# Kernel tuning notes

Hardware: AMD Instinct MI355X
Metric: run time of the kernel (lower is better)

The kernel has to match this reference:

```python
import jax, jax.numpy as jnp
import numpy as np

B, T, D_IN, H, D_ENC, P, D_ATT = 64, 20, 512, 512, 2048, 196, 512


def setup_inputs() -> dict:
    key = jax.random.key(0)
    ks = jax.random.split(key, 12)
    s = 0.05  # weight scale to keep gates out of saturation
    return {
        "x": jax.random.normal(ks[0], (B, T, D_IN), jnp.float32),
        "cnn_features": jax.random.normal(ks[1], (B, P, D_ENC), jnp.float32),
        "Wi": jax.random.normal(ks[2], (D_IN + H + D_ENC, H), jnp.float32) * s,
        "bi": jnp.zeros((H,), jnp.float32),
        "Wf": jax.random.normal(ks[3], (D_IN + H + D_ENC, H), jnp.float32) * s,
        "bf": jnp.zeros((H,), jnp.float32),
        "Wc": jax.random.normal(ks[4], (D_IN + H + D_ENC, H), jnp.float32) * s,
        "bc": jnp.zeros((H,), jnp.float32),
        "Wo": jax.random.normal(ks[5], (D_IN + H + D_ENC, H), jnp.float32) * s,
        "bo": jnp.zeros((H,), jnp.float32),
        "Wa_feat": jax.random.normal(ks[6], (D_ENC, D_ATT), jnp.float32) * s,
        "Wa_h": jax.random.normal(ks[7], (H, D_ATT), jnp.float32) * s,
        "ba": jnp.zeros((D_ATT,), jnp.float32),
        "v": jax.random.normal(ks[8], (D_ATT,), jnp.float32) * s,
    }


def reference(x, cnn_features, Wi, bi, Wf, bf, Wc, bc, Wo, bo, Wa_feat, Wa_h, ba, v):
    batch, seq_len, _ = x.shape
    hid = Wi.shape[1]
    # feature projection is h-independent: hoist out of the time loop
    feat_proj = jnp.einsum('bpe,ea->bpa', cnn_features, Wa_feat) + ba  # [B,P,A]

    def step(carry, x_t):
        h, c = carry
        # additive (Bahdanau) attention over pixels
        e = jnp.einsum('bpa,a->bp', jnp.tanh(feat_proj + (h @ Wa_h)[:, None, :]), v)
        alpha = jax.nn.softmax(e, axis=-1)                      # [B,P]
        ctx = jnp.einsum('bp,bpe->be', alpha, cnn_features)     # [B,E]
        comb = jnp.concatenate([x_t, h, ctx], axis=1)           # [B,D_IN+H+E]
        i_t = jax.nn.sigmoid(comb @ Wi + bi)
        f_t = jax.nn.sigmoid(comb @ Wf + bf)
        o_t = jax.nn.sigmoid(comb @ Wo + bo)
        c_tilde = jnp.tanh(comb @ Wc + bc)
        c_new = f_t * c + i_t * c_tilde
        h_new = o_t * jnp.tanh(c_new)
        return (h_new, c_new), h_new

    h0 = jnp.zeros((batch, hid), x.dtype)
    c0 = jnp.zeros((batch, hid), x.dtype)
    (h_T, c_T), ys = jax.lax.scan(step, (h0, c0), jnp.swapaxes(x, 0, 1))
    outputs = jnp.swapaxes(ys, 0, 1)  # [B,T,H]
    return outputs, h_T, c_T
```

## Files before the change

kernel.cpp:

```cpp
#include <hip/hip_runtime.h>

typedef unsigned short u16;
typedef unsigned int u32;
typedef __attribute__((ext_vector_type(8))) short bf16x8;
typedef __attribute__((ext_vector_type(4))) float f32x4;

#define NB 64
#define NT 20
#define NH 512
#define NP 196
#define NE 2048
#define NA 512

__device__ __forceinline__ u16 f2bf(float f) {
  u32 b = __float_as_uint(f);
  return (u16)((b + 0x7FFFu + ((b >> 16) & 1u)) >> 16);
}
__device__ __forceinline__ float bf2f(u16 u) { return __uint_as_float(((u32)u) << 16); }
__device__ __forceinline__ float tanh_fast(float x) {
  float xc = fminf(fmaxf(x, -15.f), 15.f);
  float e2 = __builtin_amdgcn_exp2f(xc * 2.885390082f);
  return (e2 - 1.f) * __builtin_amdgcn_rcpf(e2 + 1.f);
}
__device__ __forceinline__ float sigmoid_fast(float x) {
  return __builtin_amdgcn_rcpf(1.f + __builtin_amdgcn_exp2f(x * -1.44269504f));
}

__device__ __forceinline__ void gload_lds16(const u16* g, u16* l) {
  __builtin_amdgcn_global_load_lds((const __attribute__((address_space(1))) void*)g,
                                   (__attribute__((address_space(3))) void*)l, 16, 0, 0);
}

template <int N>
__device__ __forceinline__ void vwait() {
  if constexpr (N >= 0)
    asm volatile("s_waitcnt vmcnt(%0)" ::"i"(N) : "memory");
  else
    asm volatile("" ::: "memory");
}

__global__ __launch_bounds__(256) void conv_bf16(const float4* __restrict__ src,
                                                 u16* __restrict__ dst, int n4) {
  int i = blockIdx.x * 256 + threadIdx.x;
  int stride = gridDim.x * 256;
  for (; i < n4; i += stride) {
    float4 v = src[i];
    u32 lo = (u32)f2bf(v.x) | ((u32)f2bf(v.y) << 16);
    u32 hi = (u32)f2bf(v.z) | ((u32)f2bf(v.w) << 16);
    *(uint2*)(dst + (size_t)i * 4) = make_uint2(lo, hi);
  }
}

__global__ __launch_bounds__(128) void conv_x(const float* __restrict__ x,
                                              u16* __restrict__ xbT) {
  int b = blockIdx.x, t = blockIdx.y, tid = threadIdx.x;
  float4 v = *(const float4*)(x + ((size_t)b * NT + t) * 512 + tid * 4);
  u32 lo = (u32)f2bf(v.x) | ((u32)f2bf(v.y) << 16);
  u32 hi = (u32)f2bf(v.z) | ((u32)f2bf(v.w) << 16);
  *(uint2*)(xbT + ((size_t)t * NB + b) * 512 + tid * 4) = make_uint2(lo, hi);
}

__global__ __launch_bounds__(256) void transpose_w(const float* __restrict__ W0,
                                                   const float* __restrict__ W1,
                                                   const float* __restrict__ W2,
                                                   const float* __restrict__ W3,
                                                   u16* __restrict__ dst, int row_off, int K) {
  const float* src = blockIdx.z == 0 ? W0 : blockIdx.z == 1 ? W1 : blockIdx.z == 2 ? W2 : W3;
  __shared__ float tile[32][33];
  int k0 = blockIdx.x * 32, n0 = blockIdx.y * 32;
  int tx = threadIdx.x & 31, ty = threadIdx.x >> 5;
#pragma unroll
  for (int i = 0; i < 4; ++i)
    tile[ty + i * 8][tx] = src[(size_t)(row_off + k0 + ty + i * 8) * 512 + n0 + tx];
  __syncthreads();
#pragma unroll
  for (int i = 0; i < 4; ++i) {
    int n = n0 + ty + i * 8, k = k0 + tx;
    dst[((size_t)blockIdx.z * 512 + n) * K + k] = f2bf(tile[tx][ty + i * 8]);
  }
}

__global__ __launch_bounds__(256) void gemm_bf16(const u16* __restrict__ A,
                                                 const u16* __restrict__ BT,
                                                 float* __restrict__ C, int M, int N, int K) {
  __shared__ u16 lA[128 * 64];
  __shared__ u16 lB[128 * 64];
  const int tid = threadIdx.x;
  const int lane = tid & 63;
  const int wid = tid >> 6;
  const int m0 = blockIdx.x * 128, n0 = blockIdx.y * 128;
  const int wm = (wid >> 1) * 64, wn = (wid & 1) * 64;
  f32x4 acc[4][4] = {};

  const int cbase = wid * 256;
  int srcr[4], srcc[4];
#pragma unroll
  for (int it = 0; it < 4; ++it) {
    int c = cbase + it * 64 + lane;
    srcr[it] = c >> 3;
    srcc[it] = ((c & 7) ^ ((c >> 3) & 7)) * 8;
  }

  for (int k0 = 0; k0 < K; k0 += 64) {
    __syncthreads();
#pragma unroll
    for (int it = 0; it < 4; ++it) {
      gload_lds16(A + (size_t)(m0 + srcr[it]) * K + k0 + srcc[it],
                  lA + (size_t)(cbase + it * 64) * 8);
      gload_lds16(BT + (size_t)(n0 + srcr[it]) * K + k0 + srcc[it],
                  lB + (size_t)(cbase + it * 64) * 8);
    }
    __syncthreads();
#pragma unroll
    for (int kk = 0; kk < 2; ++kk) {
      int kchunk = kk * 4 + (lane >> 4);
      bf16x8 af[4], bg[4];
#pragma unroll
      for (int i = 0; i < 4; ++i) {
        int row = wm + i * 16 + (lane & 15);
        af[i] = *(const bf16x8*)(lA + row * 64 + ((kchunk ^ (row & 7)) * 8));
        int rowb = wn + i * 16 + (lane & 15);
        bg[i] = *(const bf16x8*)(lB + rowb * 64 + ((kchunk ^ (rowb & 7)) * 8));
      }
#pragma unroll
      for (int i = 0; i < 4; ++i)
#pragma unroll
        for (int j = 0; j < 4; ++j)
          acc[i][j] = __builtin_amdgcn_mfma_f32_16x16x32_bf16(af[i], bg[j], acc[i][j], 0, 0, 0);
    }
  }
#pragma unroll
  for (int i = 0; i < 4; ++i) {
    int m = m0 + wm + i * 16 + ((lane >> 4) * 4);
#pragma unroll
    for (int j = 0; j < 4; ++j) {
      int n = n0 + wn + j * 16 + (lane & 15);
#pragma unroll
      for (int r = 0; r < 4; ++r) C[(size_t)(m + r) * N + n] = acc[i][j][r];
    }
  }
}

#define STG(SS, CUR, K1)                                                                    \
  do {                                                                                      \
    _Pragma("unroll") for (int q_ = 0; q_ < 2; ++q_) {                                      \
      const u16* g_ = ((SS) < 2)                                                            \
                          ? (A + (size_t)(m0 + sR[SS][q_]) * K + (K1) + sC[SS][q_])         \
                          : (BT + (size_t)(n0 + sR[SS][q_]) * K + (K1) + sC[SS][q_]);       \
      gload_lds16(g_, lds + ((CUR) ^ 1) * 32768 + sL[SS][q_]);                              \
    }                                                                                       \
  } while (0)

#define PH(MF0, READB, CUR, DOSTAGE, SB, K1, WN)                                            \
  do {                                                                                      \
    const u16* pA_ = lds + (CUR) * 32768;                                                   \
    const u16* pB_ = pA_ + 16384;                                                           \
    bf16x8 af_[2][2];                                                                       \
    _Pragma("unroll") for (int kh_ = 0; kh_ < 2; ++kh_) {                                   \
      const int kc_ = kh_ * 4 + (lane >> 4);                                                \
      _Pragma("unroll") for (int ii_ = 0; ii_ < 2; ++ii_) {                                 \
        const int rA_ = wmH * 128 + ((MF0) + ii_) * 16 + l15;                               \
        af_[kh_][ii_] = *(const bf16x8*)(pA_ + rA_ * 64 + ((kc_ ^ (rA_ & 7)) * 8));         \
      }                                                                                     \
      if (READB) {                                                                          \
        _Pragma("unroll") for (int j_ = 0; j_ < 4; ++j_) {                                  \
          const int rB_ = wnq * 64 + j_ * 16 + l15;                                         \
          bg[kh_][j_] = *(const bf16x8*)(pB_ + rB_ * 64 + ((kc_ ^ (rB_ & 7)) * 8));         \
        }                                                                                   \
      }                                                                                     \
    }                                                                                       \
    if (DOSTAGE) {                                                                          \
      STG(SB, CUR, K1);                                                                     \
      STG((SB) + 1, CUR, K1);                                                               \
    }                                                                                       \
    vwait<WN>();                                                                            \
    __builtin_amdgcn_s_barrier();                                                           \
    __builtin_amdgcn_s_setprio(1);                                                          \
    _Pragma("unroll") for (int kh_ = 0; kh_ < 2; ++kh_)                                     \
      _Pragma("unroll") for (int ii_ = 0; ii_ < 2; ++ii_)                                   \
        _Pragma("unroll") for (int j_ = 0; j_ < 4; ++j_)                                    \
          acc[(MF0) + ii_][j_] = __builtin_amdgcn_mfma_f32_16x16x32_bf16(                   \
              af_[kh_][ii_], bg[kh_][j_], acc[(MF0) + ii_][j_], 0, 0, 0);                   \
    __builtin_amdgcn_s_setprio(0);                                                          \
    __builtin_amdgcn_s_barrier();                                                           \
  } while (0)

__global__ __launch_bounds__(512, 2) void gemm256(const u16* __restrict__ A,
                                                  const u16* __restrict__ BT,
                                                  const float* __restrict__ bias,
                                                  u16* __restrict__ fpb, u16* __restrict__ cnW,
                                                  int K, int grid_n) {
  __shared__ u16 lds[65536];
  const int tid = threadIdx.x;
  const int lane = tid & 63;
  const int wid = tid >> 6;
  const int l15 = lane & 15;
  const int nblk = gridDim.x;
  const int q = nblk >> 3, rr = nblk & 7;
  const int xcd = blockIdx.x & 7, jj = blockIdx.x >> 3;
  const int swz = (xcd < rr ? xcd * (q + 1) : rr * (q + 1) + (xcd - rr) * q) + jj;
  const int mt = swz / grid_n, nt = swz - mt * grid_n;
  const int m0 = mt * 256, n0 = nt * 256;
  const int wmH = wid >> 2;
  const int wnq = wid & 3;
  f32x4 acc[8][4] = {};
  bf16x8 bg[2][4];

  int sR[4][2], sC[4][2], sL[4][2];
#pragma unroll
  for (int s = 0; s < 4; ++s)
#pragma unroll
    for (int qq = 0; qq < 2; ++qq) {
      int reg = (s < 2) ? s : s - 2;
      int ra = reg * 1024 + qq * 512 + wid * 64;
      int idx = ra + lane;
      sR[s][qq] = idx >> 3;
      sC[s][qq] = ((idx & 7) ^ ((idx >> 3) & 7)) * 8;
      sL[s][qq] = ((s < 2) ? 0 : 16384) + ra * 8;
    }

  STG(0, 1, 0);
  STG(1, 1, 0);
  STG(2, 1, 0);
  STG(3, 1, 0);
  vwait<0>();
  __builtin_amdgcn_s_barrier();

  const int KT = K >> 6;
  for (int kt = 0; kt < KT - 1; ++kt) {
    const int cur = kt & 1;
    const int k1 = (kt + 1) << 6;
    PH(0, 1, cur, 1, 0, k1, -1);
    PH(2, 0, cur, 1, 2, k1, -1);
    PH(4, 0, cur, 0, 0, 0, -1);
    PH(6, 0, cur, 0, 0, 0, 0);
  }
  {
    const int cur = (KT - 1) & 1;
    PH(0, 1, cur, 0, 0, 0, -1);
    PH(2, 0, cur, 0, 0, 0, -1);
    PH(4, 0, cur, 0, 0, 0, -1);
    PH(6, 0, cur, 0, 0, 0, -1);
  }

#pragma unroll
  for (int i = 0; i < 8; ++i) {
    int m = m0 + wmH * 128 + i * 16 + ((lane >> 4) * 4);
#pragma unroll
    for (int j = 0; j < 4; ++j) {
      int n = n0 + wnq * 64 + j * 16 + l15;
      float bv = (n < 512) ? bias[n] : 0.f;
#pragma unroll
      for (int r = 0; r < 4; ++r) {
        float val = acc[i][j][r] + bv;
        u32 me = (u32)(m + r);
        if (n < 512) {
          fpb[(size_t)me * 512 + n] = f2bf(val);
        } else {
          u32 bdx = me / 196u;
          u32 p = me - bdx * 196u;
          u32 g = (u32)(n - 512) >> 9;
          u32 n9 = (u32)(n - 512) & 511u;
          cnW[(((size_t)bdx * 4 + g) * 196 + p) * 512 + n9] = f2bf(val);
        }
      }
    }
  }
}

__global__ __launch_bounds__(256) void hproj(const u16* __restrict__ hprev,
                                             const u16* __restrict__ wcT,
                                             float* __restrict__ hp) {
  const int ntile = blockIdx.x;
  const int tid = threadIdx.x, lane = tid & 63, kh = tid >> 6;
  const int l15 = lane & 15;
  const u16* Bp = wcT + (size_t)(ntile * 16 + l15) * 512 + kh * 128 + ((lane >> 4) * 8);
  const u16* Ap = hprev + (size_t)l15 * 512 + kh * 128 + ((lane >> 4) * 8);
  f32x4 acc[4] = {};
#pragma unroll
  for (int ks = 0; ks < 4; ++ks) {
    bf16x8 bb = *(const bf16x8*)(Bp + ks * 32);
#pragma unroll
    for (int mf = 0; mf < 4; ++mf) {
      bf16x8 a = *(const bf16x8*)(Ap + (size_t)mf * 16 * 512 + ks * 32);
      acc[mf] = __builtin_amdgcn_mfma_f32_16x16x32_bf16(a, bb, acc[mf], 0, 0, 0);
    }
  }
  __shared__ float pre[4][64][16];
  const int rrow = (lane >> 4) * 4;
#pragma unroll
  for (int mf = 0; mf < 4; ++mf)
#pragma unroll
    for (int r = 0; r < 4; ++r) pre[kh][mf * 16 + rrow + r][l15] = acc[mf][r];
  __syncthreads();
  const int m = tid >> 2, n = (tid & 3) * 4;
  float4 s;
  float* sp = (float*)&s;
#pragma unroll
  for (int j = 0; j < 4; ++j)
    sp[j] = pre[0][m][n + j] + pre[1][m][n + j] + pre[2][m][n + j] + pre[3][m][n + j];
  *(float4*)(hp + (size_t)m * 2560 + ntile * 16 + n) = s;
}

__global__ __launch_bounds__(1024) void attn_gates(
    const u16* __restrict__ fpb, const float* __restrict__ hp, const float* __restrict__ v,
    const u16* __restrict__ cw, const float* __restrict__ xw, const float* __restrict__ bi,
    const float* __restrict__ bfg, const float* __restrict__ bc, const float* __restrict__ bo,
    float* __restrict__ cbuf, float* __restrict__ out, u16* __restrict__ hnext, int t) {
  const int b = blockIdx.x & 63;
  const int quarter = blockIdx.x >> 6;
  const int tid = threadIdx.x;
  const int lane = tid & 63, wid = tid >> 6;
  __shared__ float smem_a[1024];
  __shared__ float sm[16];
  __shared__ float alp[200];
  __shared__ float red[8192];

  float* hwa = smem_a;
  float* vv = smem_a + 512;
  if (tid < 512) {
    hwa[tid] = (t > 0) ? hp[(size_t)b * 2560 + 2048 + tid] : 0.f;
    vv[tid] = v[tid];
  }
  if (tid >= 196 && tid < 256) red[tid] = -3e38f;
  __syncthreads();

  float hw[8], vr[8];
#pragma unroll
  for (int j = 0; j < 8; ++j) {
    hw[j] = hwa[lane * 8 + j];
    vr[j] = vv[lane * 8 + j];
  }
  for (int p = wid; p < NP; p += 16) {
    const u16* fp = fpb + ((size_t)b * NP + p) * 512 + lane * 8;
    uint4 raw = *(const uint4*)fp;
    u32 w[4] = {raw.x, raw.y, raw.z, raw.w};
    float part = 0.f;
#pragma unroll
    for (int j = 0; j < 8; ++j) {
      u16 u = (u16)(w[j >> 1] >> ((j & 1) * 16));
      part += tanh_fast(bf2f(u) + hw[j]) * vr[j];
    }
#pragma unroll
    for (int off = 32; off > 0; off >>= 1) part += __shfl_xor(part, off);
    if (lane == 0) red[p] = part;
  }
  __syncthreads();

  float ev = 0.f, w = 0.f;
  if (tid < 256) {
    ev = red[tid];
    float m_ = ev;
#pragma unroll
    for (int off = 32; off > 0; off >>= 1) m_ = fmaxf(m_, __shfl_xor(m_, off));
    if (lane == 0) sm[wid] = m_;
  }
  __syncthreads();
  if (tid < 256) {
    float mx = fmaxf(fmaxf(sm[0], sm[1]), fmaxf(sm[2], sm[3]));
    w = (tid < NP) ? __builtin_amdgcn_exp2f((ev - mx) * 1.44269504f) : 0.f;
    float s_ = w;
#pragma unroll
    for (int off = 32; off > 0; off >>= 1) s_ += __shfl_xor(s_, off);
    if (lane == 0) sm[8 + wid] = s_;
  }
  __syncthreads();
  if (tid < NP) {
    float tot = (sm[8] + sm[9]) + (sm[10] + sm[11]);
    alp[tid] = w * __builtin_amdgcn_rcpf(tot);
  }
  __syncthreads();

  {
    const int g = tid >> 8, pg = (tid >> 4) & 15, colc = tid & 15;
    const u16* base = cw + ((size_t)(b * 4 + g) * 196) * 512 + quarter * 128 + colc * 8;
    float acc[8] = {};
    for (int i = 0; i < 13; ++i) {
      int p = pg + i * 16;
      if (p < NP) {
        float al = alp[p];
        uint4 raw = *(const uint4*)(base + (size_t)p * 512);
        u32 wds[4] = {raw.x, raw.y, raw.z, raw.w};
#pragma unroll
        for (int j = 0; j < 8; ++j) acc[j] += al * bf2f((u16)(wds[j >> 1] >> ((j & 1) * 16)));
      }
    }
#pragma unroll
    for (int j = 0; j < 8; ++j) red[((g * 16 + pg) * 16 + colc) * 8 + j] = acc[j];
  }
  __syncthreads();

  float* pre4 = smem_a;
  if (tid < 512) {
    const int g = tid >> 7, nn = tid & 127;
    float s = 0.f;
#pragma unroll
    for (int pg = 0; pg < 16; ++pg) s += red[((g * 16 + pg) * 16 + (nn >> 3)) * 8 + (nn & 7)];
    pre4[g * 128 + nn] = s;
  }
  __syncthreads();

  if (tid < 128) {
    const int ng = quarter * 128 + tid;
    const size_t xwo = ((size_t)t * NB + b) * 2048;
    const size_t hpb = (size_t)b * 2560;
    float hwh0 = 0.f, hwh1 = 0.f, hwh2 = 0.f, hwh3 = 0.f;
    if (t > 0) {
      hwh0 = hp[hpb + ng];
      hwh1 = hp[hpb + 512 + ng];
      hwh2 = hp[hpb + 1024 + ng];
      hwh3 = hp[hpb + 1536 + ng];
    }
    float ip = pre4[0 * 128 + tid] + xw[xwo + ng] + hwh0 + bi[ng];
    float fp = pre4[1 * 128 + tid] + xw[xwo + 512 + ng] + hwh1 + bfg[ng];
    float cp = pre4[2 * 128 + tid] + xw[xwo + 1024 + ng] + hwh2 + bc[ng];
    float op = pre4[3 * 128 + tid] + xw[xwo + 1536 + ng] + hwh3 + bo[ng];
    float it = sigmoid_fast(ip), ft = sigmoid_fast(fp), ot = sigmoid_fast(op);
    float ctl = tanh_fast(cp);
    float cold = (t > 0) ? cbuf[(size_t)b * 512 + ng] : 0.f;
    float cn = ft * cold + it * ctl;
    float hn = ot * tanh_fast(cn);
    cbuf[(size_t)b * 512 + ng] = cn;
    hnext[(size_t)b * 512 + ng] = f2bf(hn);
    out[((size_t)b * NT + t) * 512 + ng] = hn;
    if (t == NT - 1) {
      out[(size_t)NB * NT * 512 + (size_t)b * 512 + ng] = hn;
      out[(size_t)NB * NT * 512 + (size_t)NB * 512 + (size_t)b * 512 + ng] = cn;
    }
  }
}

extern "C" void kernel_launch(void* const* d_in, const int* in_sizes, int n_in, void* d_out,
                              int out_size, void* d_ws, size_t ws_size, hipStream_t stream) {
  const float* x = (const float*)d_in[0];
  const float* cnn = (const float*)d_in[1];
  const float* Wi = (const float*)d_in[2];
  const float* bi = (const float*)d_in[3];
  const float* Wf = (const float*)d_in[4];
  const float* bfv = (const float*)d_in[5];
  const float* Wc = (const float*)d_in[6];
  const float* bc = (const float*)d_in[7];
  const float* Wo = (const float*)d_in[8];
  const float* bo = (const float*)d_in[9];
  const float* Waf = (const float*)d_in[10];
  const float* Wah = (const float*)d_in[11];
  const float* ba = (const float*)d_in[12];
  const float* v = (const float*)d_in[13];
  float* out = (float*)d_out;

  char* base = (char*)d_ws;
  size_t off = 0;
  auto alloc = [&](size_t bytes) {
    char* r = base + off;
    off += (bytes + 255) & ~(size_t)255;
    return r;
  };
  u16* cnnb = (u16*)alloc((size_t)NB * NP * NE * 2);
  u16* fpb = (u16*)alloc((size_t)NB * NP * NA * 2);
  u16* cnW = (u16*)alloc((size_t)NB * 4 * NP * 512 * 2);
  u16* wbig = (u16*)alloc((size_t)2560 * 2048 * 2);
  u16* wcombT = (u16*)alloc((size_t)2560 * 512 * 2);
  u16* wxt = (u16*)alloc((size_t)4 * 512 * 512 * 2);
  u16* xbT = (u16*)alloc((size_t)NT * NB * 512 * 2);
  float* xw = (float*)alloc((size_t)NT * NB * 2048 * 4);
  u16* hbuf = (u16*)alloc((size_t)2 * NB * 512 * 2);
  float* cbuf = (float*)alloc((size_t)NB * 512 * 4);
  float* hp = (float*)alloc((size_t)NB * 2560 * 4);

  (void)ws_size;
  (void)in_sizes;
  (void)n_in;
  (void)out_size;

  conv_bf16<<<2048, 256, 0, stream>>>((const float4*)cnn, cnnb, (NB * NP * NE) / 4);
  conv_x<<<dim3(NB, NT), 128, 0, stream>>>(x, xbT);
  {
    dim3 g1(512 / 32, 16, 4);
    transpose_w<<<g1, 256, 0, stream>>>(Wi, Wf, Wc, Wo, wxt, 0, 512);
    dim3 g2(2048 / 32, 16, 1);
    transpose_w<<<g2, 256, 0, stream>>>(Waf, Waf, Waf, Waf, wbig, 0, 2048);
    dim3 g3(2048 / 32, 16, 4);
    transpose_w<<<g3, 256, 0, stream>>>(Wi, Wf, Wc, Wo, wbig + (size_t)512 * 2048, 1024, 2048);
    dim3 g4(512 / 32, 16, 4);
    transpose_w<<<g4, 256, 0, stream>>>(Wi, Wf, Wc, Wo, wcombT, 512, 512);
    dim3 g5(512 / 32, 16, 1);
    transpose_w<<<g5, 256, 0, stream>>>(Wah, Wah, Wah, Wah, wcombT + (size_t)2048 * 512, 0, 512);
  }

  gemm256<<<49 * 10, 512, 0, stream>>>(cnnb, wbig, ba, fpb, cnW, 2048, 10);

  {
    dim3 g(1280 / 128, 2048 / 128);
    gemm_bf16<<<g, 256, 0, stream>>>(xbT, wxt, xw, 1280, 2048, 512);
  }

  for (int t = 0; t < NT; ++t) {
    const u16* hprev = hbuf + (size_t)(t & 1) * NB * 512;
    u16* hnext = hbuf + (size_t)((t + 1) & 1) * NB * 512;
    if (t > 0) hproj<<<160, 256, 0, stream>>>(hprev, wcombT, hp);
    attn_gates<<<256, 1024, 0, stream>>>(fpb, hp, v, cnW, xw, bi, bfv, bc, bo, cbuf, out, hnext,
                                         t);
  }
}
```

Measured before the change: 672.5 us.

## Triple-buffer A tiles and single-buffer B in gemm256 LDS pipeline

The gemm256 LDS staging moves from double-buffered A and B to a three-slot ring for A plus one B slot. A tiles are now prefetched two k-steps ahead, and B for the next step is loaded into the single slot after its fragments are read into registers in the first phase. The aim is deeper prefetch of A without growing LDS, which could hide more global-load latency. In exchange the vmcnt accounting and barrier ordering are more intricate, and the ring needs extra peeled tail iterations.

```diff
diff --git a/kernel.cpp b/kernel.cpp
--- a/kernel.cpp
+++ b/kernel.cpp
@@ -141,20 +141,26 @@
   }
 }
 
-#define STG(SS, CUR, K1)                                                                    \
+#define STGA(ABASE, K1)                                                                     \
   do {                                                                                      \
-    _Pragma("unroll") for (int q_ = 0; q_ < 2; ++q_) {                                      \
-      const u16* g_ = ((SS) < 2)                                                            \
-                          ? (A + (size_t)(m0 + sR[SS][q_]) * K + (K1) + sC[SS][q_])         \
-                          : (BT + (size_t)(n0 + sR[SS][q_]) * K + (K1) + sC[SS][q_]);       \
-      gload_lds16(g_, lds + ((CUR) ^ 1) * 32768 + sL[SS][q_]);                              \
-    }                                                                                       \
+    _Pragma("unroll") for (int s_ = 0; s_ < 2; ++s_)                                        \
+        _Pragma("unroll") for (int q_ = 0; q_ < 2; ++q_)                                    \
+            gload_lds16(A + (size_t)(m0 + sR[s_][q_]) * K + (K1) + sC[s_][q_],              \
+                        lds + (ABASE) + sL[s_][q_]);                                        \
   } while (0)
 
-#define PH(MF0, READB, CUR, DOSTAGE, SB, K1, WN)                                            \
+#define STGB(K1)                                                                            \
   do {                                                                                      \
-    const u16* pA_ = lds + (CUR) * 32768;                                                   \
-    const u16* pB_ = pA_ + 16384;                                                           \
+    _Pragma("unroll") for (int s_ = 0; s_ < 2; ++s_)                                        \
+        _Pragma("unroll") for (int q_ = 0; q_ < 2; ++q_)                                    \
+            gload_lds16(BT + (size_t)(n0 + sR[s_][q_]) * K + (K1) + sC[s_][q_],             \
+                        lds + 49152 + sL[s_][q_]);                                          \
+  } while (0)
+
+#define PH(MF0, READB, SB, WN)                                                              \
+  do {                                                                                      \
+    const u16* pA_ = lds + aoff;                                                            \
+    const u16* pB_ = lds + 49152;                                                           \
     bf16x8 af_[2][2];                                                                       \
     _Pragma("unroll") for (int kh_ = 0; kh_ < 2; ++kh_) {                                   \
       const int kc_ = kh_ * 4 + (lane >> 4);                                                \
@@ -169,10 +175,8 @@
         }                                                                                   \
       }                                                                                     \
     }                                                                                       \
-    if (DOSTAGE) {                                                                          \
-      STG(SB, CUR, K1);                                                                     \
-      STG((SB) + 1, CUR, K1);                                                               \
-    }                                                                                       \
+    if ((SB) >= 1) STGB((kt + 1) << 6);                                                     \
+    if ((SB) == 1) STGA(nxtoff, (kt + 2) << 6);                                             \
     vwait<WN>();                                                                            \
     __builtin_amdgcn_s_barrier();                                                           \
     __builtin_amdgcn_s_setprio(1);                                                          \
@@ -206,41 +210,60 @@
   f32x4 acc[8][4] = {};
   bf16x8 bg[2][4];
 
-  int sR[4][2], sC[4][2], sL[4][2];
-#pragma unroll
-  for (int s = 0; s < 4; ++s)
+  int sR[2][2], sC[2][2], sL[2][2];
+#pragma unroll
+  for (int s = 0; s < 2; ++s)
 #pragma unroll
     for (int qq = 0; qq < 2; ++qq) {
-      int reg = (s < 2) ? s : s - 2;
-      int ra = reg * 1024 + qq * 512 + wid * 64;
+      int ra = s * 1024 + qq * 512 + wid * 64;
       int idx = ra + lane;
       sR[s][qq] = idx >> 3;
       sC[s][qq] = ((idx & 7) ^ ((idx >> 3) & 7)) * 8;
-      sL[s][qq] = ((s < 2) ? 0 : 16384) + ra * 8;
-    }
-
-  STG(0, 1, 0);
-  STG(1, 1, 0);
-  STG(2, 1, 0);
-  STG(3, 1, 0);
-  vwait<0>();
+      sL[s][qq] = ra * 8;
+    }
+
+  STGA(0, 0);
+  STGB(0);
+  STGA(16384, 64);
+  vwait<4>();
   __builtin_amdgcn_s_barrier();
 
   const int KT = K >> 6;
-  for (int kt = 0; kt < KT - 1; ++kt) {
-    const int cur = kt & 1;
-    const int k1 = (kt + 1) << 6;
-    PH(0, 1, cur, 1, 0, k1, -1);
-    PH(2, 0, cur, 1, 2, k1, -1);
-    PH(4, 0, cur, 0, 0, 0, -1);
-    PH(6, 0, cur, 0, 0, 0, 0);
+  int curA = 0;
+  for (int kt = 0; kt < KT - 2; ++kt) {
+    const int aoff = curA << 14;
+    int nA = curA + 2;
+    if (nA >= 3) nA -= 3;
+    const int nxtoff = nA << 14;
+    PH(0, 1, 0, -1);
+    PH(2, 0, 1, -1);
+    PH(4, 0, 0, -1);
+    PH(6, 0, 0, 4);
+    ++curA;
+    if (curA >= 3) curA = 0;
   }
   {
-    const int cur = (KT - 1) & 1;
-    PH(0, 1, cur, 0, 0, 0, -1);
-    PH(2, 0, cur, 0, 0, 0, -1);
-    PH(4, 0, cur, 0, 0, 0, -1);
-    PH(6, 0, cur, 0, 0, 0, -1);
+    const int kt = KT - 2;
+    const int aoff = curA << 14;
+    const int nxtoff = 0;
+    (void)nxtoff;
+    PH(0, 1, 0, -1);
+    PH(2, 0, 2, -1);
+    PH(4, 0, 0, -1);
+    PH(6, 0, 0, 0);
+    ++curA;
+    if (curA >= 3) curA = 0;
+  }
+  {
+    const int kt = KT - 1;
+    (void)kt;
+    const int aoff = curA << 14;
+    const int nxtoff = 0;
+    (void)nxtoff;
+    PH(0, 1, 0, -1);
+    PH(2, 0, 0, -1);
+    PH(4, 0, 0, -1);
+    PH(6, 0, 0, -1);
   }
 
 #pragma unroll
@@ -392,11 +415,12 @@
 
   float* pre4 = smem_a;
   if (tid < 512) {
-    const int g = tid >> 7, nn = tid & 127;
+    const int gg = tid >> 7, nn = tid & 127;
     float s = 0.f;
 #pragma unroll
-    for (int pg = 0; pg < 16; ++pg) s += red[((g * 16 + pg) * 16 + (nn >> 3)) * 8 + (nn & 7)];
-    pre4[g * 128 + nn] = s;
+    for (int pg2 = 0; pg2 < 16; ++pg2)
+      s += red[((gg * 16 + pg2) * 16 + (nn >> 3)) * 8 + (nn & 7)];
+    pre4[gg * 128 + nn] = s;
   }
   __syncthreads();
 
```

New measurement: 690.4 us. +2.7%, slower.
